# Optimization experiments

Hardware: AMD Instinct MI355X
Metric: run time of the kernel (lower is better)

## Reference

```python
import jax, jax.numpy as jnp
import numpy as np

N_STEPS = 2
MAX_STEP = 1.0
EPS64 = float(np.finfo(np.float64).eps)


def _sphere_log(p, q):
    # log map on unit sphere, tangent at p pointing to q; p,q: [..., D]
    cos = jnp.clip(jnp.sum(p * q, axis=-1, keepdims=True), -1.0, 1.0)
    u = q - cos * p
    un = jnp.linalg.norm(u, axis=-1, keepdims=True)
    theta = jnp.arccos(cos)
    return theta * u / (un + 1e-12)


def _sphere_exp(p, v):
    # exp map on unit sphere; jnp.sinc(n/pi) = sin(n)/n (stable at 0)
    n = jnp.linalg.norm(v, axis=-1, keepdims=True)
    x = jnp.cos(n) * p + jnp.sinc(n / jnp.pi) * v
    return x / jnp.linalg.norm(x, axis=-1, keepdims=True)


def setup_inputs() -> dict:
    key = jax.random.key(0)
    ks = jax.random.split(key, 6)
    N, C, D, E = 50000, 16, 3, 1600000
    nodes = jax.random.normal(ks[0], (N, C, D), dtype=jnp.float32)
    nodes = nodes / jnp.linalg.norm(nodes, axis=-1, keepdims=True)  # points on S^2
    edge_w = jax.random.uniform(ks[1], (E,), dtype=jnp.float32)
    senders = jax.random.randint(ks[2], (E,), 0, N, dtype=jnp.int32)
    receivers = jax.random.randint(ks[3], (E,), 0, N, dtype=jnp.int32)
    t_sqrt = 1.0 + 0.3 * jax.random.normal(ks[4], (C,), dtype=jnp.float32)
    delta_sqrt = 1.0 + 0.3 * jax.random.normal(ks[5], (C,), dtype=jnp.float32)
    return {"nodes": nodes, "edge_w": edge_w, "t_sqrt": t_sqrt,
            "delta_sqrt": delta_sqrt, "senders": senders, "receivers": receivers}


def reference(nodes, edge_w, t_sqrt, delta_sqrt, senders, receivers):
    N = nodes.shape[0]
    t = (t_sqrt ** 2) / N_STEPS            # per-channel time, split across Euler steps
    delta = delta_sqrt ** 2                 # per-channel min step size
    deg = jax.ops.segment_sum(edge_w, senders, num_segments=N)  # [N]

    def laplace(x):
        # graph Laplacian of manifold-valued signal: weighted mean of log maps, negated
        logs = _sphere_log(x[senders], x[receivers])              # [E, C, D]
        agg = jax.ops.segment_sum(edge_w[:, None, None] * logs, senders, num_segments=N)
        return -agg / (deg[:, None, None] + 1e-12)                # [N, C, D]

    def step(x, _):
        v = laplace(x)
        nrm = jnp.sqrt(jnp.sum(v * v, axis=-1) + EPS64)           # [N, C]
        alp = jax.nn.sigmoid(nrm - delta[None, :])
        scale = jnp.where(nrm * alp <= MAX_STEP, alp, MAX_STEP / nrm)
        v = -(v * scale[..., None]) * t[None, :, None]
        return _sphere_exp(x, v), None

    x, _ = jax.lax.scan(step, nodes, None, length=N_STEPS, unroll=N_STEPS)
    return x
```

## Files before the change

kernel.cpp:

```cpp
#include <hip/hip_runtime.h>
#include <math.h>


constexpr float EPS64F = 2.2204460492503131e-16f;
constexpr float PI_F   = 3.14159265358979323846f;
constexpr int   SR_BITS = 14;
constexpr int   CH_BITS = 15;

typedef int   vi4 __attribute__((ext_vector_type(4)));
typedef float vf4 __attribute__((ext_vector_type(4)));
typedef float vf2 __attribute__((ext_vector_type(2)));


__global__ __launch_bounds__(256) void lhist_kernel(
    const int* __restrict__ snd, unsigned char* __restrict__ pos,
    int* __restrict__ partial2, int E, int NC) {
  __shared__ int h[1 << SR_BITS];
  int tid = threadIdx.x;
  int c = blockIdx.x, s = blockIdx.y;
  for (int i = tid; i < (1 << SR_BITS); i += 256) h[i] = 0;
  __syncthreads();
  int base = c << CH_BITS;
  int cnt = min(1 << CH_BITS, E - base);
  int s0 = s << SR_BITS;
  const vi4* snd4 = (const vi4*)(snd + base);
  int cnt4 = cnt >> 2;
  for (int i = tid; i < cnt4; i += 256) {
    vi4 sv = snd4[i];
    int e = base + (i << 2);
    int v;
    v = sv.x - s0; if ((unsigned)v < (1u << SR_BITS)) pos[e]     = (unsigned char)atomicAdd(&h[v], 1);
    v = sv.y - s0; if ((unsigned)v < (1u << SR_BITS)) pos[e + 1] = (unsigned char)atomicAdd(&h[v], 1);
    v = sv.z - s0; if ((unsigned)v < (1u << SR_BITS)) pos[e + 2] = (unsigned char)atomicAdd(&h[v], 1);
    v = sv.w - s0; if ((unsigned)v < (1u << SR_BITS)) pos[e + 3] = (unsigned char)atomicAdd(&h[v], 1);
  }
  if (tid == 0) {
    for (int i = cnt4 << 2; i < cnt; ++i) {
      int v = snd[base + i] - s0;
      if ((unsigned)v < (1u << SR_BITS))
        pos[base + i] = (unsigned char)atomicAdd(&h[v], 1);
    }
  }
  __syncthreads();
  int* dst = partial2 + ((size_t)(s * NC + c) << SR_BITS);
  for (int i = tid; i < (1 << SR_BITS); i += 256) dst[i] = h[i];
}

__global__ __launch_bounds__(1024) void scan1A_kernel(
    const int* __restrict__ partial2, int* __restrict__ boff,
    int* __restrict__ row_start, int* __restrict__ btot, int N, int NC) {
  __shared__ int wsum[16];
  int tid = threadIdx.x;
  int lane = tid & 63, wave = tid >> 6;
  int i = blockIdx.x * 1024 + tid;
  int v = 0;
  if (i < N) {
    int s = i >> SR_BITS, lv = i & ((1 << SR_BITS) - 1);
    int run = 0;
    for (int c = 0; c < NC; ++c) {
      int t = partial2[((size_t)(s * NC + c) << SR_BITS) + lv];
      boff[(size_t)c * N + i] = run;
      run += t;
    }
    v = run;
  }
  int incl = v;
  #pragma unroll
  for (int off = 1; off < 64; off <<= 1) {
    int t = __shfl_up(incl, off, 64);
    if (lane >= off) incl += t;
  }
  if (lane == 63) wsum[wave] = incl;
  __syncthreads();
  if (wave == 0 && lane < 16) {
    int wincl = wsum[lane];
    #pragma unroll
    for (int off = 1; off < 16; off <<= 1) {
      int t = __shfl_up(wincl, off, 64);
      if (lane >= off) wincl += t;
    }
    wsum[lane] = wincl;
  }
  __syncthreads();
  int woff = (wave > 0) ? wsum[wave - 1] : 0;
  if (i < N) row_start[i] = woff + incl - v;
  if (tid == 0) btot[blockIdx.x] = wsum[15];
}

__global__ __launch_bounds__(64) void scanB_kernel(
    const int* __restrict__ btot, int* __restrict__ boffb,
    int* __restrict__ row_start, int nb, int N) {
  int lane = threadIdx.x;
  int v = (lane < nb) ? btot[lane] : 0;
  int incl = v;
  #pragma unroll
  for (int off = 1; off < 64; off <<= 1) {
    int t = __shfl_up(incl, off, 64);
    if (lane >= off) incl += t;
  }
  if (lane < nb) boffb[lane] = incl - v;
  if (lane == 63) row_start[N] = incl;
}

__global__ __launch_bounds__(256) void scanCD_kernel(
    int* __restrict__ row_start, const int* __restrict__ boffb,
    int* __restrict__ boff, int N, int NC) {
  int i = blockIdx.x * 256 + threadIdx.x;
  if (i >= N) return;
  int rs = row_start[i] + boffb[i >> 10];
  row_start[i] = rs;
  for (int c = 0; c < NC; ++c) boff[(size_t)c * N + i] += rs;
}

__global__ __launch_bounds__(256) void fill_kernel(
    const vi4* __restrict__ snd4, const vi4* __restrict__ rcv4,
    const vf4* __restrict__ ew4, const unsigned char* __restrict__ pos,
    const int* __restrict__ boff, long long* __restrict__ pair,
    const int* __restrict__ snd, const int* __restrict__ rcv,
    const float* __restrict__ ew, int N, int E) {
  int tid = threadIdx.x;
  int E4 = E >> 2;
  #pragma unroll
  for (int gg = 0; gg < 2; ++gg) {
    int g = blockIdx.x * 512 + gg * 256 + tid;
    if (g < E4) {
      int e = g << 2;
      const int* bc = boff + (size_t)(e >> CH_BITS) * N;
      vi4 s = __builtin_nontemporal_load(&snd4[g]);
      vi4 r = __builtin_nontemporal_load(&rcv4[g]);
      vf4 w = __builtin_nontemporal_load(&ew4[g]);
      unsigned pb = *(const unsigned*)(pos + e);
      pair[bc[s.x] + (pb & 255u)] =
          (long long)(((unsigned long long)(unsigned)__float_as_int(w.x) << 32) | (unsigned)(r.x * 48));
      pair[bc[s.y] + ((pb >> 8) & 255u)] =
          (long long)(((unsigned long long)(unsigned)__float_as_int(w.y) << 32) | (unsigned)(r.y * 48));
      pair[bc[s.z] + ((pb >> 16) & 255u)] =
          (long long)(((unsigned long long)(unsigned)__float_as_int(w.z) << 32) | (unsigned)(r.z * 48));
      pair[bc[s.w] + (pb >> 24)] =
          (long long)(((unsigned long long)(unsigned)__float_as_int(w.w) << 32) | (unsigned)(r.w * 48));
    }
  }
  if (blockIdx.x == 0 && tid == 0) {
    for (int e = E4 << 2; e < E; ++e) {
      pair[boff[(size_t)(e >> CH_BITS) * N + snd[e]] + pos[e]] =
          (long long)(((unsigned long long)(unsigned)__float_as_int(ew[e]) << 32) | (unsigned)(rcv[e] * 48));
    }
    for (int z = 0; z < 16; ++z) pair[(size_t)E + z] = 0;
  }
}


__device__ __forceinline__ void edge_accum_pk(
    vf2 p0, vf2 p1, vf2 p2, vf2 q0, vf2 q1, vf2 q2, vf2 w,
    vf2& a0, vf2& a1, vf2& a2) {
  vf2 cs = p0 * q0 + p1 * q1 + p2 * q2;
  cs = __builtin_elementwise_min(vf2{1.f, 1.f},
       __builtin_elementwise_max(vf2{-1.f, -1.f}, cs));
  vf2 u0 = q0 - cs * p0;
  vf2 u1 = q1 - cs * p1;
  vf2 u2 = q2 - cs * p2;
  vf2 un2 = __builtin_elementwise_max(u0 * u0 + u1 * u1 + u2 * u2,
                                      vf2{1e-24f, 1e-24f});
  vf2 ax = __builtin_elementwise_abs(cs);
  vf2 s = __builtin_elementwise_sqrt(vf2{1.f, 1.f} - ax);
  vf2 poly = ((ax * -0.0187293f + 0.0742610f) * ax - 0.2121144f) * ax
             + 1.5707288f;
  vf2 th = s * poly;
  vf2 theta;
  theta.x = (cs.x >= 0.0f) ? th.x : (PI_F - th.x);
  theta.y = (cs.y >= 0.0f) ? th.y : (PI_F - th.y);
  vf2 rsq;
  rsq.x = __builtin_amdgcn_rsqf(un2.x);
  rsq.y = __builtin_amdgcn_rsqf(un2.y);
  vf2 coef = w * theta * rsq;
  a0 += coef * u0;
  a1 += coef * u1;
  a2 += coef * u2;
}

__device__ __forceinline__ void node_step(
    float a0, float a1, float a2, float ws, float p0, float p1, float p2,
    float ts, float dsv, float& y0, float& y1, float& y2) {
  float invdg = __builtin_amdgcn_rcpf(ws + 1e-12f);
  float g0 = a0 * invdg, g1 = a1 * invdg, g2 = a2 * invdg;
  float nrm = sqrtf(fmaf(g0, g0, fmaf(g1, g1, g2 * g2)) + EPS64F);
  float tch = ts * ts * 0.5f;
  float dch = dsv * dsv;
  float alp = __builtin_amdgcn_rcpf(1.0f + __expf(dch - nrm));
  float scale = (nrm * alp <= 1.0f) ? alp : __builtin_amdgcn_rcpf(nrm);
  float f = scale * tch;
  float v0 = g0 * f, v1 = g1 * f, v2 = g2 * f;
  float nv = sqrtf(fmaf(v0, v0, fmaf(v1, v1, v2 * v2)));
  float cn = __cosf(nv);
  float sc = (nv > 1e-20f) ? (__sinf(nv) * __builtin_amdgcn_rcpf(nv)) : 1.0f;
  float t0 = fmaf(cn, p0, sc * v0);
  float t1 = fmaf(cn, p1, sc * v1);
  float t2 = fmaf(cn, p2, sc * v2);
  float inv = __builtin_amdgcn_rsqf(fmaf(t0, t0, fmaf(t1, t1, t2 * t2)));
  y0 = t0 * inv; y1 = t1 * inv; y2 = t2 * inv;
}

__global__ __launch_bounds__(256) void flowp_kernel(
    const float* __restrict__ xin, const int* __restrict__ row_start,
    const long long* __restrict__ pair, const float* __restrict__ tsq,
    const float* __restrict__ dsq, float* __restrict__ xout, int N) {
  int node = blockIdx.x * 4 + (threadIdx.x >> 6);
  if (node >= N) return;
  int lane = threadIdx.x & 63;
  int c = lane & 15;
  int k = lane >> 4;
  int c3 = c * 3;
  int beg = row_start[node];
  int end = row_start[node + 1];
  int ip = node * 48 + c3;
  float ps0 = xin[ip], ps1 = xin[ip + 1], ps2 = xin[ip + 2];
  vf2 p0 = {ps0, ps0}, p1 = {ps1, ps1}, p2 = {ps2, ps2};
  vf2 a0 = {0.f, 0.f}, a1 = {0.f, 0.f}, a2 = {0.f, 0.f}, wsv = {0.f, 0.f};
  int iters = (end - beg + 15) >> 4;
  int j = beg + k;
  for (int t = 0; t < iters; ++t, j += 16) {
    long long e0 = __builtin_nontemporal_load(&pair[j]);
    long long e1 = __builtin_nontemporal_load(&pair[j + 4]);
    long long e2 = __builtin_nontemporal_load(&pair[j + 8]);
    long long e3 = __builtin_nontemporal_load(&pair[j + 12]);
    float w0 = (j      < end) ? __int_as_float((int)(e0 >> 32)) : 0.f;
    float w1 = (j + 4  < end) ? __int_as_float((int)(e1 >> 32)) : 0.f;
    float w2 = (j + 8  < end) ? __int_as_float((int)(e2 >> 32)) : 0.f;
    float w3 = (j + 12 < end) ? __int_as_float((int)(e3 >> 32)) : 0.f;
    const float* q0p = xin + ((int)e0 + c3);
    const float* q1p = xin + ((int)e1 + c3);
    const float* q2p = xin + ((int)e2 + c3);
    const float* q3p = xin + ((int)e3 + c3);
    float qa0 = q0p[0], qa1 = q0p[1], qa2 = q0p[2];
    float qb0 = q1p[0], qb1 = q1p[1], qb2 = q1p[2];
    float qc0 = q2p[0], qc1 = q2p[1], qc2 = q2p[2];
    float qd0 = q3p[0], qd1 = q3p[1], qd2 = q3p[2];
    vf2 wA = {w0, w1}, wB = {w2, w3};
    edge_accum_pk(p0, p1, p2, vf2{qa0, qb0}, vf2{qa1, qb1}, vf2{qa2, qb2},
                  wA, a0, a1, a2);
    edge_accum_pk(p0, p1, p2, vf2{qc0, qd0}, vf2{qc1, qd1}, vf2{qc2, qd2},
                  wB, a0, a1, a2);
    wsv += wA + wB;
  }
  float A0 = a0.x + a0.y, A1 = a1.x + a1.y, A2 = a2.x + a2.y;
  float ws = wsv.x + wsv.y;
  A0 += __shfl_xor(A0, 16); A1 += __shfl_xor(A1, 16);
  A2 += __shfl_xor(A2, 16); ws += __shfl_xor(ws, 16);
  A0 += __shfl_xor(A0, 32); A1 += __shfl_xor(A1, 32);
  A2 += __shfl_xor(A2, 32); ws += __shfl_xor(ws, 32);
  if (k == 0) {
    float y0, y1, y2;
    node_step(A0, A1, A2, ws, ps0, ps1, ps2, tsq[c], dsq[c], y0, y1, y2);
    xout[ip] = y0; xout[ip + 1] = y1; xout[ip + 2] = y2;
  }
}

static inline size_t al16(size_t x) { return (x + 15) & ~(size_t)15; }

extern "C" void kernel_launch(void* const* d_in, const int* in_sizes, int n_in,
                              void* d_out, int out_size, void* d_ws, size_t ws_size,
                              hipStream_t stream) {
  const float* nodes = (const float*)d_in[0];
  const float* ew    = (const float*)d_in[1];
  const float* tsq   = (const float*)d_in[2];
  const float* dsq   = (const float*)d_in[3];
  const int*   snd   = (const int*)d_in[4];
  const int*   rcv   = (const int*)d_in[5];
  float* out = (float*)d_out;

  int E = in_sizes[1];
  int N = in_sizes[0] / 48;

  int NS = (N + (1 << SR_BITS) - 1) >> SR_BITS;
  int NC = (E + (1 << CH_BITS) - 1) >> CH_BITS;

  size_t rsB   = al16((size_t)(N + 4) * 4);
  size_t auxB  = 512;
  size_t pairB = al16((size_t)(E + 16) * 8);
  size_t p2B   = al16(((size_t)NS * NC << SR_BITS) * 4);
  size_t boffB = al16((size_t)NC * N * 4);

  char* base = (char*)d_ws;
  int*           row_start = (int*)base;
  int*           btot      = (int*)(base + rsB);
  int*           boffb     = btot + 64;
  long long*     pair      = (long long*)(base + rsB + auxB);
  int*           partial2  = (int*)(base + rsB + auxB + pairB);
  int*           boff      = (int*)(base + rsB + auxB + pairB + p2B);
  unsigned char* pos       = (unsigned char*)(base + rsB + auxB + pairB + p2B + boffB);
  float*         xtmp      = (float*)partial2;

  int E4  = E >> 2;
  int nb  = (N + 1023) / 1024;
  int nb2 = (N + 255) / 256;
  int fbk = (E4 + 511) / 512;
  int nfb = (N + 3) / 4;

  lhist_kernel<<<dim3(NC, NS), 256, 0, stream>>>(snd, pos, partial2, E, NC);
  scan1A_kernel<<<nb, 1024, 0, stream>>>(partial2, boff, row_start, btot, N, NC);
  scanB_kernel<<<1, 64, 0, stream>>>(btot, boffb, row_start, nb, N);
  scanCD_kernel<<<nb2, 256, 0, stream>>>(row_start, boffb, boff, N, NC);
  fill_kernel<<<fbk, 256, 0, stream>>>((const vi4*)snd, (const vi4*)rcv,
                                       (const vf4*)ew, pos, boff, pair,
                                       snd, rcv, ew, N, E);

  flowp_kernel<<<nfb, 256, 0, stream>>>(nodes, row_start, pair, tsq, dsq, xtmp, N);
  flowp_kernel<<<nfb, 256, 0, stream>>>(xtmp, row_start, pair, tsq, dsq, out, N);
}
```

Measured before the change: 297.7 us.

## Pad CSR rows to multiples of 16 and drop tail bounds checks

```diff
diff --git a/kernel.cpp b/kernel.cpp
--- a/kernel.cpp
+++ b/kernel.cpp
@@ -14,7 +14,7 @@
 
 __global__ __launch_bounds__(256) void lhist_kernel(
     const int* __restrict__ snd, unsigned char* __restrict__ pos,
-    int* __restrict__ partial2, int E, int NC) {
+    unsigned char* __restrict__ partial2, int E, int NC) {
   __shared__ int h[1 << SR_BITS];
   int tid = threadIdx.x;
   int c = blockIdx.x, s = blockIdx.y;
@@ -42,18 +42,19 @@
     }
   }
   __syncthreads();
-  int* dst = partial2 + ((size_t)(s * NC + c) << SR_BITS);
-  for (int i = tid; i < (1 << SR_BITS); i += 256) dst[i] = h[i];
+  unsigned char* dst = partial2 + ((size_t)(s * NC + c) << SR_BITS);
+  for (int i = tid; i < (1 << SR_BITS); i += 256)
+    dst[i] = (unsigned char)h[i];
 }
 
 __global__ __launch_bounds__(1024) void scan1A_kernel(
-    const int* __restrict__ partial2, int* __restrict__ boff,
+    const unsigned char* __restrict__ partial2, int* __restrict__ boff,
     int* __restrict__ row_start, int* __restrict__ btot, int N, int NC) {
   __shared__ int wsum[16];
   int tid = threadIdx.x;
   int lane = tid & 63, wave = tid >> 6;
   int i = blockIdx.x * 1024 + tid;
-  int v = 0;
+  int vpad = 0;
   if (i < N) {
     int s = i >> SR_BITS, lv = i & ((1 << SR_BITS) - 1);
     int run = 0;
@@ -62,9 +63,9 @@
       boff[(size_t)c * N + i] = run;
       run += t;
     }
-    v = run;
-  }
-  int incl = v;
+    vpad = (run + 15) & ~15;
+  }
+  int incl = vpad;
   #pragma unroll
   for (int off = 1; off < 64; off <<= 1) {
     int t = __shfl_up(incl, off, 64);
@@ -83,31 +84,30 @@
   }
   __syncthreads();
   int woff = (wave > 0) ? wsum[wave - 1] : 0;
-  if (i < N) row_start[i] = woff + incl - v;
+  if (i < N) row_start[i] = woff + incl - vpad;
   if (tid == 0) btot[blockIdx.x] = wsum[15];
 }
 
-__global__ __launch_bounds__(64) void scanB_kernel(
-    const int* __restrict__ btot, int* __restrict__ boffb,
-    int* __restrict__ row_start, int nb, int N) {
-  int lane = threadIdx.x;
-  int v = (lane < nb) ? btot[lane] : 0;
-  int incl = v;
-  #pragma unroll
-  for (int off = 1; off < 64; off <<= 1) {
-    int t = __shfl_up(incl, off, 64);
-    if (lane >= off) incl += t;
-  }
-  if (lane < nb) boffb[lane] = incl - v;
-  if (lane == 63) row_start[N] = incl;
-}
-
 __global__ __launch_bounds__(256) void scanCD_kernel(
-    int* __restrict__ row_start, const int* __restrict__ boffb,
-    int* __restrict__ boff, int N, int NC) {
-  int i = blockIdx.x * 256 + threadIdx.x;
+    int* __restrict__ row_start, const int* __restrict__ btot,
+    int* __restrict__ boff, int N, int NC, int nb) {
+  __shared__ int bsh[64];
+  int tid = threadIdx.x;
+  if (tid < 64) {
+    int v = (tid < nb) ? btot[tid] : 0;
+    int incl = v;
+    #pragma unroll
+    for (int off = 1; off < 64; off <<= 1) {
+      int t = __shfl_up(incl, off, 64);
+      if (tid >= off) incl += t;
+    }
+    bsh[tid] = incl - v;
+    if (blockIdx.x == 0 && tid == 63) row_start[N] = incl;
+  }
+  __syncthreads();
+  int i = blockIdx.x * 256 + tid;
   if (i >= N) return;
-  int rs = row_start[i] + boffb[i >> 10];
+  int rs = row_start[i] + bsh[i >> 10];
   row_start[i] = rs;
   for (int c = 0; c < NC; ++c) boff[(size_t)c * N + i] += rs;
 }
@@ -145,7 +145,6 @@
       pair[boff[(size_t)(e >> CH_BITS) * N + snd[e]] + pos[e]] =
           (long long)(((unsigned long long)(unsigned)__float_as_int(ew[e]) << 32) | (unsigned)(rcv[e] * 48));
     }
-    for (int z = 0; z < 16; ++z) pair[(size_t)E + z] = 0;
   }
 }
 
@@ -200,7 +199,7 @@
   y0 = t0 * inv; y1 = t1 * inv; y2 = t2 * inv;
 }
 
-__global__ __launch_bounds__(256) void flowp_kernel(
+__global__ __launch_bounds__(256, 8) void flowp_kernel(
     const float* __restrict__ xin, const int* __restrict__ row_start,
     const long long* __restrict__ pair, const float* __restrict__ tsq,
     const float* __restrict__ dsq, float* __restrict__ xout, int N) {
@@ -216,17 +215,17 @@
   float ps0 = xin[ip], ps1 = xin[ip + 1], ps2 = xin[ip + 2];
   vf2 p0 = {ps0, ps0}, p1 = {ps1, ps1}, p2 = {ps2, ps2};
   vf2 a0 = {0.f, 0.f}, a1 = {0.f, 0.f}, a2 = {0.f, 0.f}, wsv = {0.f, 0.f};
-  int iters = (end - beg + 15) >> 4;
+  int iters = (end - beg) >> 4;
   int j = beg + k;
   for (int t = 0; t < iters; ++t, j += 16) {
     long long e0 = __builtin_nontemporal_load(&pair[j]);
     long long e1 = __builtin_nontemporal_load(&pair[j + 4]);
     long long e2 = __builtin_nontemporal_load(&pair[j + 8]);
     long long e3 = __builtin_nontemporal_load(&pair[j + 12]);
-    float w0 = (j      < end) ? __int_as_float((int)(e0 >> 32)) : 0.f;
-    float w1 = (j + 4  < end) ? __int_as_float((int)(e1 >> 32)) : 0.f;
-    float w2 = (j + 8  < end) ? __int_as_float((int)(e2 >> 32)) : 0.f;
-    float w3 = (j + 12 < end) ? __int_as_float((int)(e3 >> 32)) : 0.f;
+    float w0 = __int_as_float((int)(e0 >> 32));
+    float w1 = __int_as_float((int)(e1 >> 32));
+    float w2 = __int_as_float((int)(e2 >> 32));
+    float w3 = __int_as_float((int)(e3 >> 32));
     const float* q0p = xin + ((int)e0 + c3);
     const float* q1p = xin + ((int)e1 + c3);
     const float* q2p = xin + ((int)e2 + c3);
@@ -274,21 +273,21 @@
   int NS = (N + (1 << SR_BITS) - 1) >> SR_BITS;
   int NC = (E + (1 << CH_BITS) - 1) >> CH_BITS;
 
+  size_t padN  = (size_t)E + 15 * (size_t)N + 64;
   size_t rsB   = al16((size_t)(N + 4) * 4);
   size_t auxB  = 512;
-  size_t pairB = al16((size_t)(E + 16) * 8);
-  size_t p2B   = al16(((size_t)NS * NC << SR_BITS) * 4);
+  size_t pairB = al16(padN * 8);
+  size_t p2B   = al16((size_t)NS * NC << SR_BITS);
   size_t boffB = al16((size_t)NC * N * 4);
 
   char* base = (char*)d_ws;
   int*           row_start = (int*)base;
   int*           btot      = (int*)(base + rsB);
-  int*           boffb     = btot + 64;
   long long*     pair      = (long long*)(base + rsB + auxB);
-  int*           partial2  = (int*)(base + rsB + auxB + pairB);
+  unsigned char* partial2  = (unsigned char*)(base + rsB + auxB + pairB);
   int*           boff      = (int*)(base + rsB + auxB + pairB + p2B);
   unsigned char* pos       = (unsigned char*)(base + rsB + auxB + pairB + p2B + boffB);
-  float*         xtmp      = (float*)partial2;
+  float*         xtmp      = (float*)boff;
 
   int E4  = E >> 2;
   int nb  = (N + 1023) / 1024;
@@ -296,10 +295,10 @@
   int fbk = (E4 + 511) / 512;
   int nfb = (N + 3) / 4;
 
+  hipMemsetAsync(pair, 0, pairB, stream);
   lhist_kernel<<<dim3(NC, NS), 256, 0, stream>>>(snd, pos, partial2, E, NC);
   scan1A_kernel<<<nb, 1024, 0, stream>>>(partial2, boff, row_start, btot, N, NC);
-  scanB_kernel<<<1, 64, 0, stream>>>(btot, boffb, row_start, nb, N);
-  scanCD_kernel<<<nb2, 256, 0, stream>>>(row_start, boffb, boff, N, NC);
+  scanCD_kernel<<<nb2, 256, 0, stream>>>(row_start, btot, boff, N, NC, nb);
   fill_kernel<<<fbk, 256, 0, stream>>>((const vi4*)snd, (const vi4*)rcv,
                                        (const vf4*)ew, pos, boff, pair,
                                        snd, rcv, ew, N, E);
```

New measurement: 285.0 us. -4.3%, faster.
